# Optimization experiments

Hardware: AMD Instinct MI355X
Metric: run time of the kernel (lower is better)

## Reference

```python
import jax, jax.numpy as jnp
import numpy as np
from jax import lax

B, C, H, W = 8, 256, 128, 128


def _scan_along(x, decay, axis):
    """Linear decay recurrence s_t = decay*s_{t-1} + (1-decay)*x_t along `axis`.

    x: [B, C, H, W]; decay: [C] (constant per channel).
    """
    xm = jnp.moveaxis(x, axis, 0)          # [L, B, C, rest]
    d = decay.reshape(1, -1, 1)            # broadcast over [B, C, rest]
    one_minus_d = 1.0 - d

    def step(state, cur):
        state = d * state + one_minus_d * cur
        return state, state

    init = jnp.zeros_like(xm[0])
    _, ys = lax.scan(step, init, xm)
    return jnp.moveaxis(ys, 0, axis)


def setup_inputs() -> dict:
    key = jax.random.key(0)
    k1, k2, k3, k4 = jax.random.split(key, 4)
    x = jax.random.normal(k1, (B, C, H, W), dtype=jnp.float32)
    decay_logits = 0.5 * jax.random.normal(k2, (4, C), dtype=jnp.float32)
    mix_logits = 0.5 * jax.random.normal(k3, (4, C), dtype=jnp.float32)
    input_scale = 0.5 * jax.random.normal(k4, (4, C), dtype=jnp.float32)
    return {"x": x, "decay_logits": decay_logits,
            "mix_logits": mix_logits, "input_scale": input_scale}


def reference(x, decay_logits, mix_logits, input_scale):
    decay = jnp.clip(jax.nn.sigmoid(decay_logits), 0.05, 0.995)   # [4, C]
    mix = jax.nn.softmax(mix_logits, axis=0)                       # [4, C]
    scale = 1.0 + jnp.tanh(input_scale)                            # [4, C]

    def sc(d):  # per-channel [C] -> broadcastable [1, C, 1, 1]
        return d.reshape(1, -1, 1, 1)

    # left -> right: scan along width (axis 3)
    lr = _scan_along(x * sc(scale[0]), decay[0], axis=3)
    # right -> left: flip width, scan, flip back
    rl = jnp.flip(_scan_along(jnp.flip(x, axis=3) * sc(scale[1]), decay[1], axis=3), axis=3)
    # top -> bottom: scan along height (axis 2)
    tb = _scan_along(x * sc(scale[2]), decay[2], axis=2)
    # bottom -> top: flip height, scan, flip back
    bt = jnp.flip(_scan_along(jnp.flip(x, axis=2) * sc(scale[3]), decay[3], axis=2), axis=2)

    return sc(mix[0]) * lr + sc(mix[1]) * rl + sc(mix[2]) * tb + sc(mix[3]) * bt
```

## Files before the change

kernel.cpp:

```cpp
#include <hip/hip_runtime.h>

#define CH 256
#define HH 128
#define WW 128
#define HW (HH * WW)
#define SEGH 16
#define NSEG 8

__device__ __forceinline__ float rdlane(float v, int l) {
    return __int_as_float(__builtin_amdgcn_readlane(__float_as_int(v), l));
}
__device__ __forceinline__ float uni(float v) {
    return __int_as_float(__builtin_amdgcn_readfirstlane(__float_as_int(v)));
}

__global__ __launch_bounds__(1024, 8) void dscan_kernel(
    const float* __restrict__ x,
    const float* __restrict__ decay_logits,
    const float* __restrict__ mix_logits,
    const float* __restrict__ input_scale,
    float* __restrict__ out)
{
    extern __shared__ float smem[];
    float* __restrict__ xs  = smem;
    float* __restrict__ scr = smem + HW;

    const int img  = blockIdx.x;
    const int c    = img & (CH - 1);
    const int tid  = threadIdx.x;
    const int lane = tid & 63;

    float pv = 0.0f;
    {
        const int j = lane & 3;
        const int g = lane >> 2;
        if (g == 0) {
            const float v = decay_logits[j * CH + c];
            pv = fminf(fmaxf(1.0f / (1.0f + expf(-v)), 0.05f), 0.995f);
        } else if (g == 1) {
            const float a0 = mix_logits[0 * CH + c];
            const float a1 = mix_logits[1 * CH + c];
            const float a2 = mix_logits[2 * CH + c];
            const float a3 = mix_logits[3 * CH + c];
            const float mm = fmaxf(fmaxf(a0, a1), fmaxf(a2, a3));
            const float aj = (j == 0) ? a0 : (j == 1) ? a1 : (j == 2) ? a2 : a3;
            pv = expf(aj - mm);
        } else if (g == 2) {
            pv = 1.0f + tanhf(input_scale[j * CH + c]);
        }
    }
    const float d0 = rdlane(pv, 0), d1 = rdlane(pv, 1);
    const float d2 = rdlane(pv, 2), d3 = rdlane(pv, 3);
    const float e0 = rdlane(pv, 4), e1 = rdlane(pv, 5);
    const float e2 = rdlane(pv, 6), e3 = rdlane(pv, 7);
    const float s0 = rdlane(pv, 8), s1 = rdlane(pv, 9);
    const float s2 = rdlane(pv, 10), s3 = rdlane(pv, 11);

    const float einv = uni(1.0f / (e0 + e1 + e2 + e3));
    const float m0 = uni(e0 * einv), m1 = uni(e1 * einv);
    const float m2 = uni(e2 * einv), m3 = uni(e3 * einv);
    const float c0 = uni((1.0f - d0) * s0);
    const float c1 = uni((1.0f - d1) * s1);
    const float c2 = uni((1.0f - d2) * s2);
    const float c3 = uni((1.0f - d3) * s3);

    float p8_0, p8_1, q0[3], q1[3];
    {
        float a = d0 * d0; a = a * a;
        p8_0 = uni(a * a);
        q0[0] = uni(p8_0 * p8_0); q0[1] = uni(q0[0] * q0[0]); q0[2] = uni(q0[1] * q0[1]);
        float b = d1 * d1; b = b * b;
        p8_1 = uni(b * b);
        q1[0] = uni(p8_1 * p8_1); q1[1] = uni(q1[0] * q1[0]); q1[2] = uni(q1[1] * q1[1]);
    }
    float t2v = d2 * d2; t2v = t2v * t2v; t2v = t2v * t2v; const float d2p16 = uni(t2v * t2v);
    float t3v = d3 * d3; t3v = t3v * t3v; t3v = t3v * t3v; const float d3p16 = uni(t3v * t3v);

    const float* __restrict__ xg = x + (size_t)img * HW;
    float* __restrict__ og = out + (size_t)img * HW;

    const int col = tid & (WW - 1);
    const int seg = tid >> 7;
    const float* __restrict__ xcol = xg + seg * SEGH * WW + col;
    float xv[SEGH];

    {
        const int hr = tid >> 3;
        const int hk = tid & 7;

        const float* __restrict__ xrow = xg + hr * WW + hk * 16;
        const float4 a0 = *(const float4*)(xrow + 0);
        const float4 a1 = *(const float4*)(xrow + 4);
        const float4 a2 = *(const float4*)(xrow + 8);
        const float4 a3 = *(const float4*)(xrow + 12);
        float xr[16];
        xr[0]=a0.x;  xr[1]=a0.y;  xr[2]=a0.z;  xr[3]=a0.w;
        xr[4]=a1.x;  xr[5]=a1.y;  xr[6]=a1.z;  xr[7]=a1.w;
        xr[8]=a2.x;  xr[9]=a2.y;  xr[10]=a2.z; xr[11]=a2.w;
        xr[12]=a3.x; xr[13]=a3.y; xr[14]=a3.z; xr[15]=a3.w;

        float blo = c0 * xr[0];
#pragma unroll
        for (int i = 1; i < 8; ++i)  blo = fmaf(d0, blo, c0 * xr[i]);
        float bhi = c0 * xr[8];
#pragma unroll
        for (int i = 9; i < 16; ++i) bhi = fmaf(d0, bhi, c0 * xr[i]);
        float bL = fmaf(p8_0, blo, bhi);

        float rA = c1 * xr[15];
#pragma unroll
        for (int i = 14; i >= 8; --i) rA = fmaf(d1, rA, c1 * xr[i]);
        float rB = c1 * xr[7];
#pragma unroll
        for (int i = 6; i >= 0; --i)  rB = fmaf(d1, rB, c1 * xr[i]);
        float bR = fmaf(p8_1, rA, rB);

#pragma unroll
        for (int i = 0; i < SEGH; ++i) xv[i] = xcol[i * WW];

#pragma unroll
        for (int kk = 0; kk < 3; ++kk) {
            const int off = 1 << kk;
            const float bU = __shfl_up(bL, (unsigned)off, 8);
            bL = fmaf(q0[kk], (hk >= off) ? bU : 0.0f, bL);
            const float bD = __shfl_down(bR, (unsigned)off, 8);
            bR = fmaf(q1[kk], (hk < 8 - off) ? bD : 0.0f, bR);
        }
        float EL = __shfl_up(bL, 1u, 8);
        if (hk == 0) EL = 0.0f;
        float ER = __shfl_down(bR, 1u, 8);
        if (hk == 7) ER = 0.0f;

        float rr[16];
        float t = ER;
#pragma unroll
        for (int i = 15; i >= 0; --i) { t = fmaf(d1, t, c1 * xr[i]); rr[i] = t; }

        float l = EL;
        float* __restrict__ prow = xs + hr * WW;
#pragma unroll
        for (int j = 0; j < 4; ++j) {
            float4 o4;
            l = fmaf(d0, l, c0 * xr[4*j + 0]); o4.x = fmaf(m0, l, m1 * rr[4*j + 0]);
            l = fmaf(d0, l, c0 * xr[4*j + 1]); o4.y = fmaf(m0, l, m1 * rr[4*j + 1]);
            l = fmaf(d0, l, c0 * xr[4*j + 2]); o4.z = fmaf(m0, l, m1 * rr[4*j + 2]);
            l = fmaf(d0, l, c0 * xr[4*j + 3]); o4.w = fmaf(m0, l, m1 * rr[4*j + 3]);
            *(float4*)(prow + 4 * ((hk ^ (2*j)) + 8*j)) = o4;
        }
    }

    {
        float b2 = 0.0f;
#pragma unroll
        for (int i = 0; i < SEGH; ++i) b2 = fmaf(d2, b2, c2 * xv[i]);

        float b3 = 0.0f;
#pragma unroll
        for (int i = SEGH - 1; i >= 0; --i) b3 = fmaf(d3, b3, xv[i]);
        b3 *= c3;

        scr[tid]        = b2;
        scr[1024 + tid] = b3;
    }

    __syncthreads();

    float Sin = 0.0f;
    for (int j = 0; j < seg; ++j)
        Sin = fmaf(d2p16, Sin, scr[j * WW + col]);
    float Tin = 0.0f;
    for (int j = NSEG - 1; j > seg; --j)
        Tin = fmaf(d3p16, Tin, scr[1024 + j * WW + col]);

    {
        const int rbase = seg * SEGH;
        const int hkc = col >> 4;
        const int jc  = (col >> 2) & 3;
        const int off = 4 * ((hkc ^ (2*jc)) + 8*jc) + (col & 3);
        const float* __restrict__ pcol = xs + rbase * WW + off;

        float o[SEGH];
        float s = Sin;
#pragma unroll
        for (int i = 0; i < SEGH; ++i) {
            s = fmaf(d2, s, c2 * xv[i]);
            o[i] = fmaf(m2, s, pcol[i * WW]);
        }
        float t = Tin;
        float* __restrict__ ocol = og + rbase * WW + col;
#pragma unroll
        for (int i = SEGH - 1; i >= 0; --i) {
            t = fmaf(d3, t, c3 * xv[i]);
            ocol[i * WW] = fmaf(m3, t, o[i]);
        }
    }
}

extern "C" void kernel_launch(void* const* d_in, const int* in_sizes, int n_in,
                              void* d_out, int out_size, void* d_ws, size_t ws_size,
                              hipStream_t stream) {
    const float* x  = (const float*)d_in[0];
    const float* dl = (const float*)d_in[1];
    const float* ml = (const float*)d_in[2];
    const float* is = (const float*)d_in[3];
    float* out = (float*)d_out;

    const size_t lds_bytes = (size_t)(HW + 2048) * sizeof(float);

    static bool attr_set = false;
    if (!attr_set) {
        (void)hipFuncSetAttribute((const void*)dscan_kernel,
                                  hipFuncAttributeMaxDynamicSharedMemorySize,
                                  (int)lds_bytes);
        attr_set = true;
    }

    dim3 grid(2048), block(1024);
    hipLaunchKernelGGL(dscan_kernel, grid, block, lds_bytes, stream, x, dl, ml, is, out);
}
```

Before: 240.9 us.

## Stage input tile in LDS once, fold mix weights, use packed FMAs

```diff
diff --git a/kernel.cpp b/kernel.cpp
--- a/kernel.cpp
+++ b/kernel.cpp
@@ -7,11 +7,16 @@
 #define SEGH 16
 #define NSEG 8
 
+typedef float v2f __attribute__((ext_vector_type(2)));
+
 __device__ __forceinline__ float rdlane(float v, int l) {
     return __int_as_float(__builtin_amdgcn_readlane(__float_as_int(v), l));
 }
 __device__ __forceinline__ float uni(float v) {
     return __int_as_float(__builtin_amdgcn_readfirstlane(__float_as_int(v)));
+}
+__device__ __forceinline__ v2f pkfma(v2f a, v2f b, v2f c) {
+    return __builtin_elementwise_fma(a, b, c);
 }
 
 __global__ __launch_bounds__(1024, 8) void dscan_kernel(
@@ -30,6 +35,19 @@
     const int tid  = threadIdx.x;
     const int lane = tid & 63;
 
+    const float* __restrict__ xg = x + (size_t)img * HW;
+    float* __restrict__ og = out + (size_t)img * HW;
+
+    const int hr = tid >> 3;
+    const int hk = tid & 7;
+    float* __restrict__ prow = xs + hr * WW;
+
+    const float* __restrict__ xrow = xg + hr * WW + hk * 16;
+    const float4 a0 = *(const float4*)(xrow + 0);
+    const float4 a1 = *(const float4*)(xrow + 4);
+    const float4 a2 = *(const float4*)(xrow + 8);
+    const float4 a3 = *(const float4*)(xrow + 12);
+
     float pv = 0.0f;
     {
         const int j = lane & 3;
@@ -38,13 +56,13 @@
             const float v = decay_logits[j * CH + c];
             pv = fminf(fmaxf(1.0f / (1.0f + expf(-v)), 0.05f), 0.995f);
         } else if (g == 1) {
-            const float a0 = mix_logits[0 * CH + c];
-            const float a1 = mix_logits[1 * CH + c];
-            const float a2 = mix_logits[2 * CH + c];
-            const float a3 = mix_logits[3 * CH + c];
-            const float mm = fmaxf(fmaxf(a0, a1), fmaxf(a2, a3));
-            const float aj = (j == 0) ? a0 : (j == 1) ? a1 : (j == 2) ? a2 : a3;
-            pv = expf(aj - mm);
+            const float b0 = mix_logits[0 * CH + c];
+            const float b1 = mix_logits[1 * CH + c];
+            const float b2 = mix_logits[2 * CH + c];
+            const float b3 = mix_logits[3 * CH + c];
+            const float mm = fmaxf(fmaxf(b0, b1), fmaxf(b2, b3));
+            const float bj = (j == 0) ? b0 : (j == 1) ? b1 : (j == 2) ? b2 : b3;
+            pv = expf(bj - mm);
         } else if (g == 2) {
             pv = 1.0f + tanhf(input_scale[j * CH + c]);
         }
@@ -57,12 +75,10 @@
     const float s2 = rdlane(pv, 10), s3 = rdlane(pv, 11);
 
     const float einv = uni(1.0f / (e0 + e1 + e2 + e3));
-    const float m0 = uni(e0 * einv), m1 = uni(e1 * einv);
-    const float m2 = uni(e2 * einv), m3 = uni(e3 * einv);
-    const float c0 = uni((1.0f - d0) * s0);
-    const float c1 = uni((1.0f - d1) * s1);
-    const float c2 = uni((1.0f - d2) * s2);
-    const float c3 = uni((1.0f - d3) * s3);
+    const float c0 = uni((1.0f - d0) * s0 * (e0 * einv));
+    const float c1 = uni((1.0f - d1) * s1 * (e1 * einv));
+    const float c2 = uni((1.0f - d2) * s2 * (e2 * einv));
+    const float c3 = uni((1.0f - d3) * s3 * (e3 * einv));
 
     float p8_0, p8_1, q0[3], q1[3];
     {
@@ -76,47 +92,62 @@
     float t2v = d2 * d2; t2v = t2v * t2v; t2v = t2v * t2v; const float d2p16 = uni(t2v * t2v);
     float t3v = d3 * d3; t3v = t3v * t3v; t3v = t3v * t3v; const float d3p16 = uni(t3v * t3v);
 
-    const float* __restrict__ xg = x + (size_t)img * HW;
-    float* __restrict__ og = out + (size_t)img * HW;
+    *(float4*)(prow + 4 * ((hk ^ 0) +  0)) = a0;
+    *(float4*)(prow + 4 * ((hk ^ 2) +  8)) = a1;
+    *(float4*)(prow + 4 * ((hk ^ 4) + 16)) = a2;
+    *(float4*)(prow + 4 * ((hk ^ 6) + 24)) = a3;
+
+    float xr[16];
+    xr[0]=a0.x;  xr[1]=a0.y;  xr[2]=a0.z;  xr[3]=a0.w;
+    xr[4]=a1.x;  xr[5]=a1.y;  xr[6]=a1.z;  xr[7]=a1.w;
+    xr[8]=a2.x;  xr[9]=a2.y;  xr[10]=a2.z; xr[11]=a2.w;
+    xr[12]=a3.x; xr[13]=a3.y; xr[14]=a3.z; xr[15]=a3.w;
+
+    __syncthreads();
 
     const int col = tid & (WW - 1);
     const int seg = tid >> 7;
-    const float* __restrict__ xcol = xg + seg * SEGH * WW + col;
+    const int coff = 4 * (((col >> 4) ^ (2 * ((col >> 2) & 3))) + 8 * ((col >> 2) & 3))
+                   + (col & 3);
     float xv[SEGH];
-
-    {
-        const int hr = tid >> 3;
-        const int hk = tid & 7;
-
-        const float* __restrict__ xrow = xg + hr * WW + hk * 16;
-        const float4 a0 = *(const float4*)(xrow + 0);
-        const float4 a1 = *(const float4*)(xrow + 4);
-        const float4 a2 = *(const float4*)(xrow + 8);
-        const float4 a3 = *(const float4*)(xrow + 12);
-        float xr[16];
-        xr[0]=a0.x;  xr[1]=a0.y;  xr[2]=a0.z;  xr[3]=a0.w;
-        xr[4]=a1.x;  xr[5]=a1.y;  xr[6]=a1.z;  xr[7]=a1.w;
-        xr[8]=a2.x;  xr[9]=a2.y;  xr[10]=a2.z; xr[11]=a2.w;
-        xr[12]=a3.x; xr[13]=a3.y; xr[14]=a3.z; xr[15]=a3.w;
-
-        float blo = c0 * xr[0];
-#pragma unroll
-        for (int i = 1; i < 8; ++i)  blo = fmaf(d0, blo, c0 * xr[i]);
-        float bhi = c0 * xr[8];
-#pragma unroll
-        for (int i = 9; i < 16; ++i) bhi = fmaf(d0, bhi, c0 * xr[i]);
-        float bL = fmaf(p8_0, blo, bhi);
-
-        float rA = c1 * xr[15];
-#pragma unroll
-        for (int i = 14; i >= 8; --i) rA = fmaf(d1, rA, c1 * xr[i]);
-        float rB = c1 * xr[7];
-#pragma unroll
-        for (int i = 6; i >= 0; --i)  rB = fmaf(d1, rB, c1 * xr[i]);
-        float bR = fmaf(p8_1, rA, rB);
-
-#pragma unroll
-        for (int i = 0; i < SEGH; ++i) xv[i] = xcol[i * WW];
+    {
+        const float* __restrict__ pcol = xs + seg * SEGH * WW + coff;
+#pragma unroll
+        for (int i = 0; i < SEGH; ++i) xv[i] = pcol[i * WW];
+
+        const v2f dd23 = {d2, d3};
+        v2f b23 = {c2 * xv[0], xv[15]};
+#pragma unroll
+        for (int i = 1; i < SEGH; ++i) {
+            const v2f in = {c2 * xv[i], xv[15 - i]};
+            b23 = pkfma(dd23, b23, in);
+        }
+        scr[tid]        = b23.x;
+        scr[1024 + tid] = b23.y * c3;
+    }
+
+    __syncthreads();
+
+    float Sin = 0.0f;
+    for (int j = 0; j < seg; ++j)
+        Sin = fmaf(d2p16, Sin, scr[j * WW + col]);
+    float Tin = 0.0f;
+    for (int j = NSEG - 1; j > seg; --j)
+        Tin = fmaf(d3p16, Tin, scr[1024 + j * WW + col]);
+
+    {
+        const v2f dd01 = {d0, d1};
+        v2f pA = {c0 * xr[0], c1 * xr[7]};
+        v2f pB = {c0 * xr[8], c1 * xr[15]};
+#pragma unroll
+        for (int i = 1; i < 8; ++i) {
+            const v2f ia = {c0 * xr[i],     c1 * xr[7 - i]};
+            const v2f ib = {c0 * xr[8 + i], c1 * xr[15 - i]};
+            pA = pkfma(dd01, pA, ia);
+            pB = pkfma(dd01, pB, ib);
+        }
+        float bL = fmaf(p8_0, pA.x, pB.x);
+        float bR = fmaf(p8_1, pB.y, pA.y);
 
 #pragma unroll
         for (int kk = 0; kk < 3; ++kk) {
@@ -137,61 +168,36 @@
         for (int i = 15; i >= 0; --i) { t = fmaf(d1, t, c1 * xr[i]); rr[i] = t; }
 
         float l = EL;
-        float* __restrict__ prow = xs + hr * WW;
 #pragma unroll
         for (int j = 0; j < 4; ++j) {
             float4 o4;
-            l = fmaf(d0, l, c0 * xr[4*j + 0]); o4.x = fmaf(m0, l, m1 * rr[4*j + 0]);
-            l = fmaf(d0, l, c0 * xr[4*j + 1]); o4.y = fmaf(m0, l, m1 * rr[4*j + 1]);
-            l = fmaf(d0, l, c0 * xr[4*j + 2]); o4.z = fmaf(m0, l, m1 * rr[4*j + 2]);
-            l = fmaf(d0, l, c0 * xr[4*j + 3]); o4.w = fmaf(m0, l, m1 * rr[4*j + 3]);
+            l = fmaf(d0, l, c0 * xr[4*j + 0]); o4.x = l + rr[4*j + 0];
+            l = fmaf(d0, l, c0 * xr[4*j + 1]); o4.y = l + rr[4*j + 1];
+            l = fmaf(d0, l, c0 * xr[4*j + 2]); o4.z = l + rr[4*j + 2];
+            l = fmaf(d0, l, c0 * xr[4*j + 3]); o4.w = l + rr[4*j + 3];
             *(float4*)(prow + 4 * ((hk ^ (2*j)) + 8*j)) = o4;
         }
     }
 
-    {
-        float b2 = 0.0f;
-#pragma unroll
-        for (int i = 0; i < SEGH; ++i) b2 = fmaf(d2, b2, c2 * xv[i]);
-
-        float b3 = 0.0f;
-#pragma unroll
-        for (int i = SEGH - 1; i >= 0; --i) b3 = fmaf(d3, b3, xv[i]);
-        b3 *= c3;
-
-        scr[tid]        = b2;
-        scr[1024 + tid] = b3;
-    }
-
     __syncthreads();
 
-    float Sin = 0.0f;
-    for (int j = 0; j < seg; ++j)
-        Sin = fmaf(d2p16, Sin, scr[j * WW + col]);
-    float Tin = 0.0f;
-    for (int j = NSEG - 1; j > seg; --j)
-        Tin = fmaf(d3p16, Tin, scr[1024 + j * WW + col]);
-
     {
         const int rbase = seg * SEGH;
-        const int hkc = col >> 4;
-        const int jc  = (col >> 2) & 3;
-        const int off = 4 * ((hkc ^ (2*jc)) + 8*jc) + (col & 3);
-        const float* __restrict__ pcol = xs + rbase * WW + off;
+        const float* __restrict__ pcol = xs + rbase * WW + coff;
 
         float o[SEGH];
         float s = Sin;
 #pragma unroll
         for (int i = 0; i < SEGH; ++i) {
             s = fmaf(d2, s, c2 * xv[i]);
-            o[i] = fmaf(m2, s, pcol[i * WW]);
+            o[i] = s + pcol[i * WW];
         }
         float t = Tin;
         float* __restrict__ ocol = og + rbase * WW + col;
 #pragma unroll
         for (int i = SEGH - 1; i >= 0; --i) {
             t = fmaf(d3, t, c3 * xv[i]);
-            ocol[i * WW] = fmaf(m3, t, o[i]);
+            ocol[i * WW] = t + o[i];
         }
     }
 }
```

Result: slower. 309.1 us (+28.3%).
